# Kernel tuning notes

Hardware: AMD Instinct MI355X
Metric: run time of the kernel (lower is better)

Reference implementation:

```python
import math
import jax, jax.numpy as jnp
import numpy as np

D_MODEL = 1024
NHEAD = 16
NUM_TEMP = 4
HEAD = D_MODEL // NHEAD          # 64
DIM = HEAD // NUM_TEMP           # 16
SCALE = math.sqrt(HEAD)
B, L = 2, 2048


def _make_freq():
    # freq = 10000^(-arange(0,dim,2)/dim), repeat_interleave(2) -> length DIM
    f = np.power(10000.0, -np.arange(0, DIM, 2) / DIM)
    return jnp.asarray(np.repeat(f, 2), dtype=jnp.float32)  # (DIM,)


def setup_inputs() -> dict:
    key = jax.random.key(0)
    ks = jax.random.split(key, 8)
    s = 0.02
    return {
        "data": jax.random.normal(ks[0], (B, L, D_MODEL), jnp.float32),
        "temporal": jax.random.uniform(ks[1], (B, L, NUM_TEMP), jnp.float32),
        "mask": jnp.zeros((L, L), jnp.float32),
        "Wq": jax.random.normal(ks[2], (D_MODEL, D_MODEL), jnp.float32) * s,
        "bq": jnp.zeros((D_MODEL,), jnp.float32),
        "Wk": jax.random.normal(ks[3], (D_MODEL, D_MODEL), jnp.float32) * s,
        "bk": jnp.zeros((D_MODEL,), jnp.float32),
        "Wv": jax.random.normal(ks[4], (D_MODEL, D_MODEL), jnp.float32) * s,
        "bv": jnp.zeros((D_MODEL,), jnp.float32),
    }


def _rotate_half_pairs(x):
    # [-x2, x1, -x4, x3, ...] along last dim
    stacked = jnp.stack([-x[..., 1::2], x[..., 0::2]], axis=-1)
    return stacked.reshape(x.shape)


def _apply_rotary(x, sine, cosine):
    # x: (B,L,H,HEAD); sine/cosine: (B,L,HEAD)
    return x * cosine[:, :, None, :] + _rotate_half_pairs(x) * sine[:, :, None, :]


def reference(data, temporal, mask, Wq, bq, Wk, bk, Wv, bv):
    freq = _make_freq()  # (DIM,)
    b, l, _ = data.shape
    q = (data @ Wq + bq).reshape(b, l, NHEAD, HEAD)
    k = (data @ Wk + bk).reshape(b, l, NHEAD, HEAD)
    v = (data @ Wv + bv).reshape(b, l, NHEAD, HEAD)
    # per-temporal-column frequencies: (B,L,T,DIM) -> (B,L,HEAD)
    freqs = (temporal[..., None] * freq).reshape(b, l, HEAD)
    cosine = jnp.cos(freqs)
    sine = jnp.sin(freqs)
    rq = _apply_rotary(q, sine, cosine)
    rk = _apply_rotary(k, sine, cosine)
    logits = jnp.einsum("bqhs,bkhs->bhqk", rq, rk) / SCALE + mask
    weights = jax.nn.softmax(logits, axis=-1)  # dropout is identity at eval
    context = jnp.einsum("bhqk,bkhs->bqhs", weights, v)
    return context.reshape(b, l, D_MODEL)
```

## Files before the change

### kernel.cpp

```cpp
#include <hip/hip_runtime.h>
#include <hip/hip_bf16.h>

#define LSEQ 2048
#define DM   1024
#define NH   16

typedef __attribute__((ext_vector_type(8)))  short bf16x8;
typedef __attribute__((ext_vector_type(8)))  unsigned short u16x8;
typedef __attribute__((ext_vector_type(4)))  float f32x4;
typedef __attribute__((ext_vector_type(16))) float f32x16;
typedef __attribute__((ext_vector_type(4)))  unsigned int u32x4;

#define LOG2E 1.4426950408889634f
#define C1SC  0.18033688011112042f

static __device__ __forceinline__ float exp2fast(float x) {
  return __builtin_amdgcn_exp2f(x);
}

static __device__ __forceinline__ unsigned short f2bf(float f) {
  unsigned int u = __float_as_uint(f);
  u += 0x7FFFu + ((u >> 16) & 1u);
  return (unsigned short)(u >> 16);
}

static __device__ __forceinline__ unsigned pk2(float a, float b) {
  __hip_bfloat162 t = __float22bfloat162_rn(make_float2(a, b));
  return *reinterpret_cast<unsigned*>(&t);
}

static __device__ __forceinline__ f32x16 unpack16(u16x8 a, u16x8 b) {
  const u32x4 ua = __builtin_bit_cast(u32x4, a);
  const u32x4 ub = __builtin_bit_cast(u32x4, b);
  f32x16 r;
#pragma unroll
  for (int i = 0; i < 4; ++i) {
    r[2 * i]     = __uint_as_float(ua[i] << 16);
    r[2 * i + 1] = __uint_as_float(ua[i] & 0xFFFF0000u);
    r[8 + 2 * i]     = __uint_as_float(ub[i] << 16);
    r[8 + 2 * i + 1] = __uint_as_float(ub[i] & 0xFFFF0000u);
  }
  return r;
}

static __device__ __forceinline__ bf16x8 pack8(const f32x16& s, int base) {
  u32x4 w;
  w[0] = pk2(s[base + 0], s[base + 1]); w[1] = pk2(s[base + 2], s[base + 3]);
  w[2] = pk2(s[base + 4], s[base + 5]); w[3] = pk2(s[base + 6], s[base + 7]);
  return __builtin_bit_cast(bf16x8, w);
}

static __device__ __forceinline__ void gld_lds16(const unsigned short* g, unsigned short* l) {
  __builtin_amdgcn_global_load_lds(
      (const __attribute__((address_space(1))) unsigned int*)g,
      (__attribute__((address_space(3))) unsigned int*)l, 16, 0, 0);
}

__global__ void k_convert_data(const float* __restrict__ src,
                               unsigned short* __restrict__ dst, int n4) {
  int i = blockIdx.x * 256 + threadIdx.x;
  if (i >= n4) return;
  float4 v = reinterpret_cast<const float4*>(src)[i];
  ushort4 o;
  o.x = f2bf(v.x); o.y = f2bf(v.y); o.z = f2bf(v.z); o.w = f2bf(v.w);
  reinterpret_cast<ushort4*>(dst)[i] = o;
}

__global__ void k_transpose_w(const float* __restrict__ Wq,
                              const float* __restrict__ Wk,
                              const float* __restrict__ Wv,
                              unsigned short* __restrict__ Wt) {
  __shared__ unsigned short tile[64][65];
  const float* W = (blockIdx.z == 0) ? Wq : (blockIdx.z == 1) ? Wk : Wv;
  int n0 = blockIdx.x * 64, k0 = blockIdx.y * 64;
  int t = threadIdx.x;
  int c = t & 63, r0 = t >> 6;
  for (int i = 0; i < 16; ++i) {
    int r = r0 + i * 4;
    tile[r][c] = f2bf(W[(size_t)(k0 + r) * DM + n0 + c]);
  }
  __syncthreads();
  size_t nbase = (size_t)blockIdx.z * DM + n0;
  for (int i = 0; i < 16; ++i) {
    int n = r0 + i * 4;
    Wt[(nbase + n) * DM + k0 + c] = tile[c][n];
  }
}

__global__ void k_maskC(const float* __restrict__ mask,
                        unsigned short* __restrict__ maskCb,
                        int* __restrict__ zflags) {
  __shared__ float tile[64][65];
  __shared__ int nz;
  int q0 = blockIdx.x * 64, kv0 = blockIdx.y * 64;
  int t = threadIdx.x;
  if (t == 0) nz = 0;
  __syncthreads();
  int c = t & 63, r0 = t >> 6;
  int lnz = 0;
  for (int i = 0; i < 16; ++i) {
    int r = r0 + i * 4;
    float v = mask[(size_t)(q0 + r) * LSEQ + kv0 + c];
    tile[r][c] = v;
    lnz |= (v != 0.0f);
  }
  if (lnz) atomicOr(&nz, 1);
  __syncthreads();
  const int q = t & 63, slot = t >> 6;
  const int tt = slot >> 1, hh = slot & 1;
  u16x8 va, vb;
#pragma unroll
  for (int r = 0; r < 8; ++r) {
    const int kvloc = 32 * tt + 4 * hh + (r & 3) + 8 * (r >> 2);
    va[r] = f2bf(tile[q][kvloc] * LOG2E);
  }
#pragma unroll
  for (int r = 8; r < 16; ++r) {
    const int kvloc = 32 * tt + 4 * hh + (r & 3) + 8 * (r >> 2);
    vb[r - 8] = f2bf(tile[q][kvloc] * LOG2E);
  }
  unsigned short* dst = maskCb + ((size_t)((kv0 >> 6) * 4 + slot) * 2048 + q0 + q) * 16;
  *reinterpret_cast<u16x8*>(dst) = va;
  *reinterpret_cast<u16x8*>(dst + 8) = vb;
  if (t == 0) zflags[blockIdx.y * 32 + blockIdx.x] = (nz == 0);
}

__global__ __launch_bounds__(256) void k_qkv_gemm(
    const unsigned short* __restrict__ A, const unsigned short* __restrict__ Bt,
    const float* __restrict__ bq, const float* __restrict__ bk,
    const float* __restrict__ bv, const float* __restrict__ temporal,
    unsigned short* __restrict__ qbuf, unsigned short* __restrict__ kbuf,
    unsigned short* __restrict__ vtbuf) {
  __shared__ unsigned short As[128 * 32];
  __shared__ unsigned short Bs[128 * 32];
  __shared__ unsigned short otile[128 * 136];
  const int tid = threadIdx.x;
  const int lane = tid & 63, wid = tid >> 6;
  const int wm = wid >> 1, wn = wid & 1;
  const int lr = lane & 15, lg = lane >> 4;

  const int bid = blockIdx.x;
  const int xcd = bid & 7, rr = bid >> 3;
  const int mblk = xcd * 4 + (rr / 24);
  const int nblk = rr % 24;
  const int m0 = mblk * 128;
  const int n0 = nblk * 128;

  f32x4 acc[4][4] = {};

  const int e0 = tid * 8;
  const int e1 = (256 + tid) * 8;
  const int ra0 = e0 >> 5, ca0 = e0 & 31;
  const int ra1 = e1 >> 5, ca1 = e1 & 31;
  unsigned short* lA0 = As + wid * 512;
  unsigned short* lA1 = As + 2048 + wid * 512;
  unsigned short* lB0 = Bs + wid * 512;
  unsigned short* lB1 = Bs + 2048 + wid * 512;

  for (int k0 = 0; k0 < DM; k0 += 32) {
    __syncthreads();
    gld_lds16(A + (size_t)(m0 + ra0) * DM + k0 + ca0, lA0);
    gld_lds16(A + (size_t)(m0 + ra1) * DM + k0 + ca1, lA1);
    gld_lds16(Bt + (size_t)(n0 + ra0) * DM + k0 + ca0, lB0);
    gld_lds16(Bt + (size_t)(n0 + ra1) * DM + k0 + ca1, lB1);
    __syncthreads();
    bf16x8 af[4], bfv[4];
    for (int mi = 0; mi < 4; ++mi)
      af[mi] = *reinterpret_cast<const bf16x8*>(As + (wm * 64 + mi * 16 + lr) * 32 + lg * 8);
    for (int ni = 0; ni < 4; ++ni)
      bfv[ni] = *reinterpret_cast<const bf16x8*>(Bs + (wn * 64 + ni * 16 + lr) * 32 + lg * 8);
    for (int mi = 0; mi < 4; ++mi)
      for (int ni = 0; ni < 4; ++ni)
        acc[mi][ni] = __builtin_amdgcn_mfma_f32_16x16x32_bf16(af[mi], bfv[ni], acc[mi][ni], 0, 0, 0);
  }

  const int mat = n0 >> 10;
  const int c0 = n0 & 1023;
  const int bb = m0 >> 11;
  const int mloc = m0 & 2047;
  const float qscale = (mat == 0) ? C1SC : 1.f;

  for (int mi = 0; mi < 4; ++mi) {
    const int rrel_base = wm * 64 + mi * 16 + lg * 4;
    for (int ni = 0; ni < 4; ++ni) {
      const int crel = wn * 64 + ni * 16 + lr;
      const int c = (c0 + crel);
      const int d = c & 63;
      const float bias = (mat == 0 ? bq : mat == 1 ? bk : bv)[c];
      f32x4 v = acc[mi][ni];
      if (mat < 2) {
        const int jj = d & 15, tt = d >> 4;
        const float fr = __expf(-(float)(jj & 14) * 0.5756462732485115f);
        const float sign = (d & 1) ? 1.f : -1.f;
        for (int j = 0; j < 4; ++j) {
          const int rrel = rrel_base + j;
          const float x = v[j] + bias;
          const float part = __shfl_xor(x, 1, 64);
          const int lqs = mloc + rrel;
          const float fq = temporal[((size_t)bb * LSEQ + lqs) * 4 + tt] * fr;
          float sn, cs;
          __sincosf(fq, &sn, &cs);
          otile[rrel * 136 + crel] = f2bf((x * cs + sign * part * sn) * qscale);
        }
      } else {
        for (int j = 0; j < 4; ++j) {
          const int rrel = rrel_base + j;
          otile[crel * 136 + rrel] = f2bf(v[j] + bias);
        }
      }
    }
  }
  __syncthreads();

  for (int i = 0; i < 2; ++i) {
    const int h = (c0 >> 6) + i;
    const size_t bh = (size_t)(bb * NH + h);
    if (mat == 0) {
      const size_t base = (bh * LSEQ + mloc) * 64;
#pragma unroll
      for (int kk2 = 0; kk2 < 4; ++kk2) {
        const int e = kk2 * 2048 + tid * 8;
        const int r = e >> 6, d = e & 63;
        *reinterpret_cast<u16x8*>(qbuf + base + e) =
            *reinterpret_cast<const u16x8*>(otile + r * 136 + i * 64 + d);
      }
    } else if (mat == 1) {
      const size_t base = bh * 131072 + (size_t)(mloc >> 5) * 2048;
#pragma unroll
      for (int kk2 = 0; kk2 < 4; ++kk2) {
        const int e = kk2 * 2048 + tid * 8;
        const int r = kk2 * 32 + ((tid >> 1) & 31);
        const int d = ((tid >> 6) & 3) * 16 + (tid & 1) * 8;
        *reinterpret_cast<u16x8*>(kbuf + base + e) =
            *reinterpret_cast<const u16x8*>(otile + r * 136 + i * 64 + d);
      }
    } else {
      const size_t base = bh * 131072 + (size_t)(mloc >> 4) * 1024;
#pragma unroll
      for (int kk2 = 0; kk2 < 4; ++kk2) {
        const int e = kk2 * 2048 + tid * 8;
        const int d = ((tid >> 6) & 1) * 32 + ((tid >> 1) & 31);
        const int rb = (kk2 * 2 + (tid >> 7)) * 16;
        const int dl = (tid & 1) * 4;
        const unsigned short* srow = otile + (i * 64 + d) * 136 + rb + dl;
        ushort4 lo = *reinterpret_cast<const ushort4*>(srow);
        ushort4 hi4 = *reinterpret_cast<const ushort4*>(srow + 8);
        u16x8 w;
        w[0] = lo.x; w[1] = lo.y; w[2] = lo.z; w[3] = lo.w;
        w[4] = hi4.x; w[5] = hi4.y; w[6] = hi4.z; w[7] = hi4.w;
        *reinterpret_cast<u16x8*>(vtbuf + base + e) = w;
      }
    }
  }
}

__global__ __launch_bounds__(256) void k_attn(
    const unsigned short* __restrict__ qbuf, const unsigned short* __restrict__ kbuf,
    const unsigned short* __restrict__ vtbuf, const unsigned short* __restrict__ maskCb,
    const int* __restrict__ zflags, float* __restrict__ out) {
  __shared__ float obuf[2][64][68];
  __shared__ float mlbuf[4][2][32][2];
  const int tid = threadIdx.x, lane = tid & 63, wid = tid >> 6;
  const int lq = lane & 31, hi = lane >> 5;
  const int qh = wid & 1, kvh = wid >> 1;

  const int bid = blockIdx.x;
  const int xcd = bid & 7, loc = bid >> 3;
  const int bh = xcd * 4 + (loc >> 4);
  const int qblk = loc & 15;

  const int q0 = qblk * 128 + qh * 64;
  const int qgA = q0 + lq, qgB = q0 + 32 + lq;
  const size_t bhL = (size_t)bh * LSEQ;
  const unsigned short* kb = kbuf + (size_t)bh * 131072;
  const unsigned short* vb = vtbuf + (size_t)bh * 131072;
  const unsigned short* mbA = maskCb + ((size_t)hi * 2048 + qgA) * 16;
  const unsigned short* mbB = maskCb + ((size_t)hi * 2048 + qgB) * 16;

  bf16x8 qfA[4], qfB[4];
#pragma unroll
  for (int c = 0; c < 4; ++c) {
    qfA[c] = *reinterpret_cast<const bf16x8*>(qbuf + (bhL + qgA) * 64 + c * 16 + hi * 8);
    qfB[c] = *reinterpret_cast<const bf16x8*>(qbuf + (bhL + qgB) * 64 + c * 16 + hi * 8);
  }

  f32x16 oA0 = {}, oA1 = {}, oB0 = {}, oB1 = {};
  float m2 = 2.0f, lA = 0.f, lB = 0.f;

  const int kv_beg = kvh * 1024, kv_end = kv_beg + 1024;
  for (int kv0 = kv_beg; kv0 < kv_end; kv0 += 64) {
    f32x16 sA0, sA1, sB0, sB1;
    const int zf = zflags[(kv0 >> 6) * 32 + (q0 >> 6)];
    if (zf) {
      sA0 = (f32x16){}; sA1 = (f32x16){};
      sB0 = (f32x16){}; sB1 = (f32x16){};
    } else {
      const size_t mo = (size_t)(kv0 >> 6) * (4 * 2048 * 16);
      const unsigned short* mtA = mbA + mo;
      const unsigned short* mtB = mbB + mo;
      sA0 = unpack16(*reinterpret_cast<const u16x8*>(mtA),
                     *reinterpret_cast<const u16x8*>(mtA + 8));
      sA1 = unpack16(*reinterpret_cast<const u16x8*>(mtA + 2 * 2048 * 16),
                     *reinterpret_cast<const u16x8*>(mtA + 2 * 2048 * 16 + 8));
      sB0 = unpack16(*reinterpret_cast<const u16x8*>(mtB),
                     *reinterpret_cast<const u16x8*>(mtB + 8));
      sB1 = unpack16(*reinterpret_cast<const u16x8*>(mtB + 2 * 2048 * 16),
                     *reinterpret_cast<const u16x8*>(mtB + 2 * 2048 * 16 + 8));
    }

    const unsigned short* kch = kb + (size_t)(kv0 >> 5) * 2048;
#pragma unroll
    for (int c = 0; c < 4; ++c) {
      bf16x8 k0 = *reinterpret_cast<const bf16x8*>(kch + c * 512 + lq * 16 + hi * 8);
      bf16x8 k1 = *reinterpret_cast<const bf16x8*>(kch + 2048 + c * 512 + lq * 16 + hi * 8);
      sA0 = __builtin_amdgcn_mfma_f32_32x32x16_bf16(k0, qfA[c], sA0, 0, 0, 0);
      sB0 = __builtin_amdgcn_mfma_f32_32x32x16_bf16(k0, qfB[c], sB0, 0, 0, 0);
      sA1 = __builtin_amdgcn_mfma_f32_32x32x16_bf16(k1, qfA[c], sA1, 0, 0, 0);
      sB1 = __builtin_amdgcn_mfma_f32_32x32x16_bf16(k1, qfB[c], sB1, 0, 0, 0);
    }

    const unsigned short* vch = vb + (size_t)(kv0 >> 4) * 1024;
    bf16x8 vf[8];
#pragma unroll
    for (int ks = 0; ks < 4; ++ks) {
      vf[2 * ks]     = *reinterpret_cast<const bf16x8*>(vch + ks * 1024 + lq * 16 + hi * 8);
      vf[2 * ks + 1] = *reinterpret_cast<const bf16x8*>(vch + ks * 1024 + 512 + lq * 16 + hi * 8);
    }

    float a0 = 0.f, a1 = 0.f, b0 = 0.f, b1 = 0.f;
#pragma unroll
    for (int r = 0; r < 8; ++r) {
      sA0[r] = exp2fast(sA0[r] - m2);     a0 += sA0[r];
      sA0[r + 8] = exp2fast(sA0[r + 8] - m2); a1 += sA0[r + 8];
      sB0[r] = exp2fast(sB0[r] - m2);     b0 += sB0[r];
      sB0[r + 8] = exp2fast(sB0[r + 8] - m2); b1 += sB0[r + 8];
    }
#pragma unroll
    for (int r = 0; r < 8; ++r) {
      sA1[r] = exp2fast(sA1[r] - m2);     a0 += sA1[r];
      sA1[r + 8] = exp2fast(sA1[r + 8] - m2); a1 += sA1[r + 8];
      sB1[r] = exp2fast(sB1[r] - m2);     b0 += sB1[r];
      sB1[r + 8] = exp2fast(sB1[r + 8] - m2); b1 += sB1[r + 8];
    }
    float rsA = a0 + a1, rsB = b0 + b1;

    if (__any(fmaxf(rsA, rsB) > 2048.f)) {
      const float cc = 0.000244140625f;
#pragma unroll
      for (int r = 0; r < 16; ++r) {
        sA0[r] *= cc; sA1[r] *= cc; sB0[r] *= cc; sB1[r] *= cc;
        oA0[r] *= cc; oA1[r] *= cc; oB0[r] *= cc; oB1[r] *= cc;
      }
      rsA *= cc; rsB *= cc; lA *= cc; lB *= cc;
      m2 += 12.f;
    }

    rsA += __shfl_xor(rsA, 32, 64);
    rsB += __shfl_xor(rsB, 32, 64);
    lA += rsA; lB += rsB;

    bf16x8 pfA0 = pack8(sA0, 0), pfA1 = pack8(sA0, 8);
    bf16x8 pfA2 = pack8(sA1, 0), pfA3 = pack8(sA1, 8);
    bf16x8 pfB0 = pack8(sB0, 0), pfB1 = pack8(sB0, 8);
    bf16x8 pfB2 = pack8(sB1, 0), pfB3 = pack8(sB1, 8);

#pragma unroll
    for (int ks = 0; ks < 4; ++ks) {
      bf16x8 pfA = (ks == 0) ? pfA0 : (ks == 1) ? pfA1 : (ks == 2) ? pfA2 : pfA3;
      bf16x8 pfB = (ks == 0) ? pfB0 : (ks == 1) ? pfB1 : (ks == 2) ? pfB2 : pfB3;
      oA0 = __builtin_amdgcn_mfma_f32_32x32x16_bf16(vf[2 * ks], pfA, oA0, 0, 0, 0);
      oB0 = __builtin_amdgcn_mfma_f32_32x32x16_bf16(vf[2 * ks], pfB, oB0, 0, 0, 0);
      oA1 = __builtin_amdgcn_mfma_f32_32x32x16_bf16(vf[2 * ks + 1], pfA, oA1, 0, 0, 0);
      oB1 = __builtin_amdgcn_mfma_f32_32x32x16_bf16(vf[2 * ks + 1], pfB, oB1, 0, 0, 0);
    }
  }

  if (lane < 32) {
    mlbuf[wid][0][lq][0] = m2; mlbuf[wid][0][lq][1] = lA;
    mlbuf[wid][1][lq][0] = m2; mlbuf[wid][1][lq][1] = lB;
  }
  __syncthreads();
  const int pw = wid ^ 2;
  const float mAp = mlbuf[pw][0][lq][0], lAp = mlbuf[pw][0][lq][1];
  const float mBp = mlbuf[pw][1][lq][0], lBp = mlbuf[pw][1][lq][1];
  const float msA = fmaxf(m2, mAp);
  const float fA = exp2fast(m2 - msA), fAp = exp2fast(mAp - msA);
  const float scaleA = fA / (lA * fA + lAp * fAp);
  const float msB = fmaxf(m2, mBp);
  const float fB = exp2fast(m2 - msB), fBp = exp2fast(mBp - msB);
  const float scaleB = fB / (lB * fB + lBp * fBp);

  if (kvh == 0) {
#pragma unroll
    for (int g = 0; g < 4; ++g) {
      const int d0 = 8 * g + 4 * hi;
      float4 wA0 = make_float4(oA0[4 * g] * scaleA, oA0[4 * g + 1] * scaleA,
                               oA0[4 * g + 2] * scaleA, oA0[4 * g + 3] * scaleA);
      float4 wA1 = make_float4(oA1[4 * g] * scaleA, oA1[4 * g + 1] * scaleA,
                               oA1[4 * g + 2] * scaleA, oA1[4 * g + 3] * scaleA);
      float4 wB0 = make_float4(oB0[4 * g] * scaleB, oB0[4 * g + 1] * scaleB,
                               oB0[4 * g + 2] * scaleB, oB0[4 * g + 3] * scaleB);
      float4 wB1 = make_float4(oB1[4 * g] * scaleB, oB1[4 * g + 1] * scaleB,
                               oB1[4 * g + 2] * scaleB, oB1[4 * g + 3] * scaleB);
      *reinterpret_cast<float4*>(&obuf[qh][lq][d0])           = wA0;
      *reinterpret_cast<float4*>(&obuf[qh][lq][d0 + 32])      = wA1;
      *reinterpret_cast<float4*>(&obuf[qh][32 + lq][d0])      = wB0;
      *reinterpret_cast<float4*>(&obuf[qh][32 + lq][d0 + 32]) = wB1;
    }
  }
  __syncthreads();
  if (kvh == 1) {
    const int b = bh >> 4, h = bh & 15;
    float* orowA = out + (size_t)(b * LSEQ + qgA) * DM + h * 64;
    float* orowB = out + (size_t)(b * LSEQ + qgB) * DM + h * 64;
#pragma unroll
    for (int g = 0; g < 4; ++g) {
      const int d0 = 8 * g + 4 * hi;
      float4 pA0 = *reinterpret_cast<const float4*>(&obuf[qh][lq][d0]);
      float4 pA1 = *reinterpret_cast<const float4*>(&obuf[qh][lq][d0 + 32]);
      float4 pB0 = *reinterpret_cast<const float4*>(&obuf[qh][32 + lq][d0]);
      float4 pB1 = *reinterpret_cast<const float4*>(&obuf[qh][32 + lq][d0 + 32]);
      float4 wA0 = make_float4(pA0.x + oA0[4 * g] * scaleA, pA0.y + oA0[4 * g + 1] * scaleA,
                               pA0.z + oA0[4 * g + 2] * scaleA, pA0.w + oA0[4 * g + 3] * scaleA);
      float4 wA1 = make_float4(pA1.x + oA1[4 * g] * scaleA, pA1.y + oA1[4 * g + 1] * scaleA,
                               pA1.z + oA1[4 * g + 2] * scaleA, pA1.w + oA1[4 * g + 3] * scaleA);
      float4 wB0 = make_float4(pB0.x + oB0[4 * g] * scaleB, pB0.y + oB0[4 * g + 1] * scaleB,
                               pB0.z + oB0[4 * g + 2] * scaleB, pB0.w + oB0[4 * g + 3] * scaleB);
      float4 wB1 = make_float4(pB1.x + oB1[4 * g] * scaleB, pB1.y + oB1[4 * g + 1] * scaleB,
                               pB1.z + oB1[4 * g + 2] * scaleB, pB1.w + oB1[4 * g + 3] * scaleB);
      *reinterpret_cast<float4*>(orowA + d0)      = wA0;
      *reinterpret_cast<float4*>(orowA + d0 + 32) = wA1;
      *reinterpret_cast<float4*>(orowB + d0)      = wB0;
      *reinterpret_cast<float4*>(orowB + d0 + 32) = wB1;
    }
  }
}

extern "C" void kernel_launch(void* const* d_in, const int* in_sizes, int n_in,
                              void* d_out, int out_size, void* d_ws, size_t ws_size,
                              hipStream_t stream) {
  const float* data     = (const float*)d_in[0];
  const float* temporal = (const float*)d_in[1];
  const float* mask     = (const float*)d_in[2];
  const float* Wq       = (const float*)d_in[3];
  const float* bq       = (const float*)d_in[4];
  const float* Wk       = (const float*)d_in[5];
  const float* bk       = (const float*)d_in[6];
  const float* Wv       = (const float*)d_in[7];
  const float* bv       = (const float*)d_in[8];
  float* out = (float*)d_out;

  char* ws = (char*)d_ws;
  unsigned short* data_bf = (unsigned short*)(ws);
  unsigned short* wt      = (unsigned short*)(ws + (size_t)8  * 1048576);
  unsigned short* qbuf    = (unsigned short*)(ws + (size_t)14 * 1048576);
  unsigned short* kbuf    = (unsigned short*)(ws + (size_t)22 * 1048576);
  unsigned short* vtbuf   = (unsigned short*)(ws + (size_t)30 * 1048576);
  unsigned short* maskCb  = data_bf;
  int* zflags             = (int*)wt;

  hipLaunchKernelGGL(k_convert_data, dim3(4096), dim3(256), 0, stream,
                     data, data_bf, (2 * LSEQ * DM) / 4);
  hipLaunchKernelGGL(k_transpose_w, dim3(16, 16, 3), dim3(256), 0, stream,
                     Wq, Wk, Wv, wt);
  hipLaunchKernelGGL(k_qkv_gemm, dim3(768), dim3(256), 0, stream,
                     data_bf, wt, bq, bk, bv, temporal, qbuf, kbuf, vtbuf);
  hipLaunchKernelGGL(k_maskC, dim3(32, 32), dim3(256), 0, stream,
                     mask, maskCb, zflags);
  hipLaunchKernelGGL(k_attn, dim3(512), dim3(256), 0, stream,
                     qbuf, kbuf, vtbuf, maskCb, zflags, out);
}
```

Baseline: 132.3 us.

## Software-pipeline attention loop over 32-key halves with QK/softmax overlap

Restructures the attention inner loop to process 32-key halves, double-buffering K fragments and overlapping the next half's QK MFMAs with the current half's softmax and PV MFMAs. It folds the max subtraction into the MFMA accumulator init (mask minus m2), defers the cross-lane row-sum shuffle to after the loop, and adds s_setprio around MFMA groups plus a launch-bounds occupancy hint of 2. The aim is to hide exp/pack latency and global-load latency behind matrix work, at the cost of more register pressure, a rescale check run twice as often, and a redundant final K prefetch.

```diff
diff --git a/kernel.cpp b/kernel.cpp
--- a/kernel.cpp
+++ b/kernel.cpp
@@ -254,7 +254,7 @@
   }
 }
 
-__global__ __launch_bounds__(256) void k_attn(
+__global__ __launch_bounds__(256, 2) void k_attn(
     const unsigned short* __restrict__ qbuf, const unsigned short* __restrict__ kbuf,
     const unsigned short* __restrict__ vtbuf, const unsigned short* __restrict__ maskCb,
     const int* __restrict__ zflags, float* __restrict__ out) {
@@ -276,6 +276,10 @@
   const unsigned short* vb = vtbuf + (size_t)bh * 131072;
   const unsigned short* mbA = maskCb + ((size_t)hi * 2048 + qgA) * 16;
   const unsigned short* mbB = maskCb + ((size_t)hi * 2048 + qgB) * 16;
+  const int lqh16 = lq * 16 + hi * 8;
+  const int kv_beg = kvh * 1024;
+  const int hk_base = kv_beg >> 5;
+  const int hv_base = kv_beg >> 4;
 
   bf16x8 qfA[4], qfB[4];
 #pragma unroll
@@ -285,95 +289,121 @@
   }
 
   f32x16 oA0 = {}, oA1 = {}, oB0 = {}, oB1 = {};
-  float m2 = 2.0f, lA = 0.f, lB = 0.f;
-
-  const int kv_beg = kvh * 1024, kv_end = kv_beg + 1024;
-  for (int kv0 = kv_beg; kv0 < kv_end; kv0 += 64) {
-    f32x16 sA0, sA1, sB0, sB1;
-    const int zf = zflags[(kv0 >> 6) * 32 + (q0 >> 6)];
-    if (zf) {
-      sA0 = (f32x16){}; sA1 = (f32x16){};
-      sB0 = (f32x16){}; sB1 = (f32x16){};
-    } else {
-      const size_t mo = (size_t)(kv0 >> 6) * (4 * 2048 * 16);
-      const unsigned short* mtA = mbA + mo;
-      const unsigned short* mtB = mbB + mo;
-      sA0 = unpack16(*reinterpret_cast<const u16x8*>(mtA),
-                     *reinterpret_cast<const u16x8*>(mtA + 8));
-      sA1 = unpack16(*reinterpret_cast<const u16x8*>(mtA + 2 * 2048 * 16),
-                     *reinterpret_cast<const u16x8*>(mtA + 2 * 2048 * 16 + 8));
-      sB0 = unpack16(*reinterpret_cast<const u16x8*>(mtB),
-                     *reinterpret_cast<const u16x8*>(mtB + 8));
-      sB1 = unpack16(*reinterpret_cast<const u16x8*>(mtB + 2 * 2048 * 16),
-                     *reinterpret_cast<const u16x8*>(mtB + 2 * 2048 * 16 + 8));
+  float m2 = 2.0f, lA_loc = 0.f, lB_loc = 0.f;
+  f32x16 cinit;
+#pragma unroll
+  for (int r = 0; r < 16; ++r) cinit[r] = -m2;
+
+#define LOADK(KF, H) {                                                         \
+    const unsigned short* kch = kb + (size_t)(hk_base + (H)) * 2048;           \
+    KF[0] = *reinterpret_cast<const bf16x8*>(kch + lqh16);                     \
+    KF[1] = *reinterpret_cast<const bf16x8*>(kch + 512 + lqh16);               \
+    KF[2] = *reinterpret_cast<const bf16x8*>(kch + 1024 + lqh16);              \
+    KF[3] = *reinterpret_cast<const bf16x8*>(kch + 1536 + lqh16);              \
+  }
+
+#define LOADV(VF, H) {                                                         \
+    const unsigned short* vch = vb + (size_t)(hv_base + 2 * (H)) * 1024;       \
+    VF[0] = *reinterpret_cast<const bf16x8*>(vch + lqh16);                     \
+    VF[1] = *reinterpret_cast<const bf16x8*>(vch + 512 + lqh16);               \
+    VF[2] = *reinterpret_cast<const bf16x8*>(vch + 1024 + lqh16);              \
+    VF[3] = *reinterpret_cast<const bf16x8*>(vch + 1536 + lqh16);              \
+  }
+
+#define QKSTEP(SA, SB, KF, H) {                                                \
+    const int kv32 = kv_beg + 32 * (H);                                        \
+    const int zf = zflags[(kv32 >> 6) * 32 + (q0 >> 6)];                       \
+    __builtin_amdgcn_s_setprio(1);                                             \
+    if (zf) {                                                                  \
+      SA = __builtin_amdgcn_mfma_f32_32x32x16_bf16(KF[0], qfA[0], cinit, 0, 0, 0); \
+      SB = __builtin_amdgcn_mfma_f32_32x32x16_bf16(KF[0], qfB[0], cinit, 0, 0, 0); \
+    } else {                                                                   \
+      const size_t mo = (size_t)((kv32 >> 6) * 4 + ((kv32 >> 5) & 1) * 2) * 32768; \
+      const unsigned short* mtA = mbA + mo;                                    \
+      const unsigned short* mtB = mbB + mo;                                    \
+      f32x16 cA = unpack16(*reinterpret_cast<const u16x8*>(mtA),               \
+                           *reinterpret_cast<const u16x8*>(mtA + 8));          \
+      f32x16 cB = unpack16(*reinterpret_cast<const u16x8*>(mtB),               \
+                           *reinterpret_cast<const u16x8*>(mtB + 8));          \
+      _Pragma("unroll")                                                        \
+      for (int r = 0; r < 16; ++r) { cA[r] -= m2; cB[r] -= m2; }               \
+      SA = __builtin_amdgcn_mfma_f32_32x32x16_bf16(KF[0], qfA[0], cA, 0, 0, 0); \
+      SB = __builtin_amdgcn_mfma_f32_32x32x16_bf16(KF[0], qfB[0], cB, 0, 0, 0); \
+    }                                                                          \
+    _Pragma("unroll")                                                          \
+    for (int c = 1; c < 4; ++c) {                                              \
+      SA = __builtin_amdgcn_mfma_f32_32x32x16_bf16(KF[c], qfA[c], SA, 0, 0, 0); \
+      SB = __builtin_amdgcn_mfma_f32_32x32x16_bf16(KF[c], qfB[c], SB, 0, 0, 0); \
+    }                                                                          \
+    __builtin_amdgcn_s_setprio(0);                                             \
+  }
+
+#define SMAX_PV(SA, SB, VF) {                                                  \
+    float a0 = 0.f, a1 = 0.f, b0 = 0.f, b1 = 0.f;                              \
+    _Pragma("unroll")                                                          \
+    for (int r = 0; r < 8; ++r) {                                              \
+      SA[r] = exp2fast(SA[r]);         a0 += SA[r];                            \
+      SA[r + 8] = exp2fast(SA[r + 8]); a1 += SA[r + 8];                        \
+      SB[r] = exp2fast(SB[r]);         b0 += SB[r];                            \
+      SB[r + 8] = exp2fast(SB[r + 8]); b1 += SB[r + 8];                        \
+    }                                                                          \
+    float rsA = a0 + a1, rsB = b0 + b1;                                        \
+    if (__any(fmaxf(rsA, rsB) > 2048.f)) {                                     \
+      const float cc = 0.000244140625f;                                        \
+      _Pragma("unroll")                                                        \
+      for (int r = 0; r < 16; ++r) {                                           \
+        SA[r] *= cc; SB[r] *= cc;                                              \
+        oA0[r] *= cc; oA1[r] *= cc; oB0[r] *= cc; oB1[r] *= cc;                \
+      }                                                                        \
+      rsA *= cc; rsB *= cc; lA_loc *= cc; lB_loc *= cc;                        \
+      m2 += 12.f;                                                              \
+      _Pragma("unroll")                                                        \
+      for (int r = 0; r < 16; ++r) cinit[r] = -m2;                             \
+    }                                                                          \
+    lA_loc += rsA; lB_loc += rsB;                                              \
+    bf16x8 pA0 = pack8(SA, 0), pB0 = pack8(SB, 0);                             \
+    bf16x8 pA1 = pack8(SA, 8), pB1 = pack8(SB, 8);                             \
+    __builtin_amdgcn_s_setprio(1);                                             \
+    oA0 = __builtin_amdgcn_mfma_f32_32x32x16_bf16(VF[0], pA0, oA0, 0, 0, 0);   \
+    oB0 = __builtin_amdgcn_mfma_f32_32x32x16_bf16(VF[0], pB0, oB0, 0, 0, 0);   \
+    oA1 = __builtin_amdgcn_mfma_f32_32x32x16_bf16(VF[1], pA0, oA1, 0, 0, 0);   \
+    oB1 = __builtin_amdgcn_mfma_f32_32x32x16_bf16(VF[1], pB0, oB1, 0, 0, 0);   \
+    oA0 = __builtin_amdgcn_mfma_f32_32x32x16_bf16(VF[2], pA1, oA0, 0, 0, 0);   \
+    oB0 = __builtin_amdgcn_mfma_f32_32x32x16_bf16(VF[2], pB1, oB0, 0, 0, 0);   \
+    oA1 = __builtin_amdgcn_mfma_f32_32x32x16_bf16(VF[3], pA1, oA1, 0, 0, 0);   \
+    oB1 = __builtin_amdgcn_mfma_f32_32x32x16_bf16(VF[3], pB1, oB1, 0, 0, 0);   \
+    __builtin_amdgcn_s_setprio(0);                                             \
+  }
+
+  bf16x8 kf0[4], kf1[4], vf[4];
+  f32x16 s0A, s0B, s1A, s1B;
+
+  LOADK(kf0, 0);
+  QKSTEP(s0A, s0B, kf0, 0);
+  LOADK(kf1, 1);
+
+#pragma unroll 1
+  for (int i = 0; i < 16; ++i) {
+    const int h = 2 * i;
+    {
+      const int hp = (h + 2 < 32) ? h + 2 : 31;
+      LOADK(kf0, hp);
+      LOADV(vf, h);
+      QKSTEP(s1A, s1B, kf1, h + 1);
+      SMAX_PV(s0A, s0B, vf);
     }
-
-    const unsigned short* kch = kb + (size_t)(kv0 >> 5) * 2048;
-#pragma unroll
-    for (int c = 0; c < 4; ++c) {
-      bf16x8 k0 = *reinterpret_cast<const bf16x8*>(kch + c * 512 + lq * 16 + hi * 8);
-      bf16x8 k1 = *reinterpret_cast<const bf16x8*>(kch + 2048 + c * 512 + lq * 16 + hi * 8);
-      sA0 = __builtin_amdgcn_mfma_f32_32x32x16_bf16(k0, qfA[c], sA0, 0, 0, 0);
-      sB0 = __builtin_amdgcn_mfma_f32_32x32x16_bf16(k0, qfB[c], sB0, 0, 0, 0);
-      sA1 = __builtin_amdgcn_mfma_f32_32x32x16_bf16(k1, qfA[c], sA1, 0, 0, 0);
-      sB1 = __builtin_amdgcn_mfma_f32_32x32x16_bf16(k1, qfB[c], sB1, 0, 0, 0);
+    {
+      const int hp = (h + 3 < 32) ? h + 3 : 31;
+      const int hq = (h + 2 < 32) ? h + 2 : 31;
+      LOADK(kf1, hp);
+      LOADV(vf, h + 1);
+      QKSTEP(s0A, s0B, kf0, hq);
+      SMAX_PV(s1A, s1B, vf);
     }
-
-    const unsigned short* vch = vb + (size_t)(kv0 >> 4) * 1024;
-    bf16x8 vf[8];
-#pragma unroll
-    for (int ks = 0; ks < 4; ++ks) {
-      vf[2 * ks]     = *reinterpret_cast<const bf16x8*>(vch + ks * 1024 + lq * 16 + hi * 8);
-      vf[2 * ks + 1] = *reinterpret_cast<const bf16x8*>(vch + ks * 1024 + 512 + lq * 16 + hi * 8);
-    }
-
-    float a0 = 0.f, a1 = 0.f, b0 = 0.f, b1 = 0.f;
-#pragma unroll
-    for (int r = 0; r < 8; ++r) {
-      sA0[r] = exp2fast(sA0[r] - m2);     a0 += sA0[r];
-      sA0[r + 8] = exp2fast(sA0[r + 8] - m2); a1 += sA0[r + 8];
-      sB0[r] = exp2fast(sB0[r] - m2);     b0 += sB0[r];
-      sB0[r + 8] = exp2fast(sB0[r + 8] - m2); b1 += sB0[r + 8];
-    }
-#pragma unroll
-    for (int r = 0; r < 8; ++r) {
-      sA1[r] = exp2fast(sA1[r] - m2);     a0 += sA1[r];
-      sA1[r + 8] = exp2fast(sA1[r + 8] - m2); a1 += sA1[r + 8];
-      sB1[r] = exp2fast(sB1[r] - m2);     b0 += sB1[r];
-      sB1[r + 8] = exp2fast(sB1[r + 8] - m2); b1 += sB1[r + 8];
-    }
-    float rsA = a0 + a1, rsB = b0 + b1;
-
-    if (__any(fmaxf(rsA, rsB) > 2048.f)) {
-      const float cc = 0.000244140625f;
-#pragma unroll
-      for (int r = 0; r < 16; ++r) {
-        sA0[r] *= cc; sA1[r] *= cc; sB0[r] *= cc; sB1[r] *= cc;
-        oA0[r] *= cc; oA1[r] *= cc; oB0[r] *= cc; oB1[r] *= cc;
-      }
-      rsA *= cc; rsB *= cc; lA *= cc; lB *= cc;
-      m2 += 12.f;
-    }
-
-    rsA += __shfl_xor(rsA, 32, 64);
-    rsB += __shfl_xor(rsB, 32, 64);
-    lA += rsA; lB += rsB;
-
-    bf16x8 pfA0 = pack8(sA0, 0), pfA1 = pack8(sA0, 8);
-    bf16x8 pfA2 = pack8(sA1, 0), pfA3 = pack8(sA1, 8);
-    bf16x8 pfB0 = pack8(sB0, 0), pfB1 = pack8(sB0, 8);
-    bf16x8 pfB2 = pack8(sB1, 0), pfB3 = pack8(sB1, 8);
-
-#pragma unroll
-    for (int ks = 0; ks < 4; ++ks) {
-      bf16x8 pfA = (ks == 0) ? pfA0 : (ks == 1) ? pfA1 : (ks == 2) ? pfA2 : pfA3;
-      bf16x8 pfB = (ks == 0) ? pfB0 : (ks == 1) ? pfB1 : (ks == 2) ? pfB2 : pfB3;
-      oA0 = __builtin_amdgcn_mfma_f32_32x32x16_bf16(vf[2 * ks], pfA, oA0, 0, 0, 0);
-      oB0 = __builtin_amdgcn_mfma_f32_32x32x16_bf16(vf[2 * ks], pfB, oB0, 0, 0, 0);
-      oA1 = __builtin_amdgcn_mfma_f32_32x32x16_bf16(vf[2 * ks + 1], pfA, oA1, 0, 0, 0);
-      oB1 = __builtin_amdgcn_mfma_f32_32x32x16_bf16(vf[2 * ks + 1], pfB, oB1, 0, 0, 0);
-    }
-  }
+  }
+
+  const float lA = lA_loc + __shfl_xor(lA_loc, 32, 64);
+  const float lB = lB_loc + __shfl_xor(lB_loc, 32, 64);
 
   if (lane < 32) {
     mlbuf[wid][0][lq][0] = m2; mlbuf[wid][0][lq][1] = lA;
@@ -434,6 +464,10 @@
       *reinterpret_cast<float4*>(orowB + d0 + 32) = wB1;
     }
   }
+#undef LOADK
+#undef LOADV
+#undef QKSTEP
+#undef SMAX_PV
 }
 
 extern "C" void kernel_launch(void* const* d_in, const int* in_sizes, int n_in,
```

New measurement: 141.0 us. 6.6% more time.
